# Kernel optimization log

Hardware: AMD Instinct MI355X
Metric: run time of the kernel (lower is better)

The kernel has to match this reference:

```python
import jax, jax.numpy as jnp
import numpy as np

P_ASEM = 0.6


def setup_inputs() -> dict:
    key = jax.random.key(0)
    k1, k2, k3 = jax.random.split(key, 3)
    B, N, D = 8, 2048, 512
    x = jax.random.normal(k1, (B, N, D), dtype=jnp.float32)
    adj = jax.random.uniform(k2, (B, N, N), dtype=jnp.float32)
    # nn.Linear(2D, 1): weight [1, 2D], bias [1]
    bound = 1.0 / np.sqrt(2 * D)
    W = jax.random.uniform(k3, (1, 2 * D), dtype=jnp.float32, minval=-bound, maxval=bound)
    b = jnp.zeros((1,), dtype=jnp.float32)
    return {"x": x, "adj": adj, "W": W, "b": b}


def reference(x, adj, W, b):
    # Faithful to: sigmoid(Linear(cat(xi, xj))) with xi=x[:, i], xj=x[:, j].
    # Split W = [Wi | Wj] so Linear(cat) = x_i @ Wi.T + x_j @ Wj.T + b,
    # avoiding the O(B*N^2*2D) concat intermediate.
    D = x.shape[-1]
    Wi = W[:, :D]  # [1, D]
    Wj = W[:, D:]  # [1, D]
    si = jnp.einsum('bnd,d->bn', x, Wi[0])  # [B, N]
    sj = jnp.einsum('bnd,d->bn', x, Wj[0])  # [B, N]
    xij = jax.nn.sigmoid(si[:, :, None] + sj[:, None, :] + b[0])  # [B, N, N]
    return P_ASEM * xij + (1.0 - P_ASEM) * adj
```

## Files before the change

### kernel.cpp

```cpp
#include <hip/hip_runtime.h>
#include <hip/hip_bf16.h>

#define PB 8
#define PN 2048
#define PD 512
#define P_ASEM 0.6f

typedef float v4f __attribute__((ext_vector_type(4)));

__global__ __launch_bounds__(256) void row_dots_kernel(
    const float* __restrict__ x,
    const float* __restrict__ W,
    float* __restrict__ si,
    float* __restrict__ sj)
{
    const int wave = threadIdx.x >> 6;
    const int lane = threadIdx.x & 63;
    const int row  = blockIdx.x * 4 + wave;

    const v4f* xr = (const v4f*)(x + (size_t)row * PD);
    const v4f* Wi = (const v4f*)(W);
    const v4f* Wj = (const v4f*)(W + PD);

    v4f a0  = __builtin_nontemporal_load(xr + lane);
    v4f a1  = __builtin_nontemporal_load(xr + lane + 64);
    v4f wi0 = Wi[lane];
    v4f wi1 = Wi[lane + 64];
    v4f wj0 = Wj[lane];
    v4f wj1 = Wj[lane + 64];

    float acc_i = a0.x*wi0.x + a0.y*wi0.y + a0.z*wi0.z + a0.w*wi0.w
                + a1.x*wi1.x + a1.y*wi1.y + a1.z*wi1.z + a1.w*wi1.w;
    float acc_j = a0.x*wj0.x + a0.y*wj0.y + a0.z*wj0.z + a0.w*wj0.w
                + a1.x*wj1.x + a1.y*wj1.y + a1.z*wj1.z + a1.w*wj1.w;

    #pragma unroll
    for (int off = 32; off > 0; off >>= 1) {
        acc_i += __shfl_down(acc_i, off, 64);
        acc_j += __shfl_down(acc_j, off, 64);
    }
    if (lane == 0) {
        si[row] = acc_i;
        sj[row] = acc_j;
    }
}

__device__ __forceinline__ float fsigmoid(float t) {
    return __frcp_rn(1.0f + __expf(-t));
}

__global__ __launch_bounds__(256) void blend_kernel(
    const float* __restrict__ adj,
    const float* __restrict__ si,
    const float* __restrict__ sj,
    const float* __restrict__ bptr,
    float* __restrict__ out)
{
    const size_t base = (size_t)blockIdx.x * 1024 + threadIdx.x;
    const float bias = bptr[0];

    size_t idx[4];
    v4f av[4];
    #pragma unroll
    for (int k = 0; k < 4; ++k) {
        idx[k] = base + (size_t)k * 256;
        av[k] = __builtin_nontemporal_load((const v4f*)adj + idx[k]);
    }

    #pragma unroll
    for (int k = 0; k < 4; ++k) {
        const int row  = (int)(idx[k] >> 9);
        const int jc   = (int)(idx[k] & 511);
        const int bidx = row >> 11;
        const float s  = si[row] + bias;
        const v4f sv   = ((const v4f*)(sj + (size_t)bidx * PN))[jc];

        v4f r;
        r.x = P_ASEM * fsigmoid(s + sv.x) + (1.0f - P_ASEM) * av[k].x;
        r.y = P_ASEM * fsigmoid(s + sv.y) + (1.0f - P_ASEM) * av[k].y;
        r.z = P_ASEM * fsigmoid(s + sv.z) + (1.0f - P_ASEM) * av[k].z;
        r.w = P_ASEM * fsigmoid(s + sv.w) + (1.0f - P_ASEM) * av[k].w;
        __builtin_nontemporal_store(r, (v4f*)out + idx[k]);
    }
}

extern "C" void kernel_launch(void* const* d_in, const int* in_sizes, int n_in,
                              void* d_out, int out_size, void* d_ws, size_t ws_size,
                              hipStream_t stream) {
    const float* x   = (const float*)d_in[0];
    const float* adj = (const float*)d_in[1];
    const float* W   = (const float*)d_in[2];
    const float* b   = (const float*)d_in[3];
    float* out = (float*)d_out;

    float* si = (float*)d_ws;
    float* sj = si + (PB * PN);

    row_dots_kernel<<<(PB * PN) / 4, 256, 0, stream>>>(x, W, si, sj);

    const size_t nblocks = (size_t)PB * PN * PN / 4 / 1024;
    blend_kernel<<<(int)nblocks, 256, 0, stream>>>(adj, si, sj, b, out);
}
```

Measured before the change: 242.5 us.

## Factor sigmoid exponentials per row/column and process four rows per block

Sigmoid(si+sj+b) is rewritten as 1/(1+exp(-si-b)*exp(-sj)), so the exponentials are computed once per row and column in the row-dot kernel. The blend kernel then needs only an FMA and a hardware reciprocal per element. Each block now covers four full rows with eight loads per thread, and reuses the column factors across those rows, cutting per-element index math and exp work. The product of two exponentials can overflow or underflow for large logits, and the raw rcp is less exact than before. The kernel remains bound by memory bandwidth on adj and out.

```diff
diff --git a/kernel.cpp b/kernel.cpp
--- a/kernel.cpp
+++ b/kernel.cpp
@@ -1,5 +1,4 @@
 #include <hip/hip_runtime.h>
-#include <hip/hip_bf16.h>
 
 #define PB 8
 #define PN 2048
@@ -11,8 +10,9 @@
 __global__ __launch_bounds__(256) void row_dots_kernel(
     const float* __restrict__ x,
     const float* __restrict__ W,
-    float* __restrict__ si,
-    float* __restrict__ sj)
+    const float* __restrict__ bptr,
+    float* __restrict__ esi,
+    float* __restrict__ esj)
 {
     const int wave = threadIdx.x >> 6;
     const int lane = threadIdx.x & 63;
@@ -40,48 +40,54 @@
         acc_j += __shfl_down(acc_j, off, 64);
     }
     if (lane == 0) {
-        si[row] = acc_i;
-        sj[row] = acc_j;
+        esi[row] = __expf(-(acc_i + bptr[0]));
+        esj[row] = __expf(-acc_j);
     }
 }
 
-__device__ __forceinline__ float fsigmoid(float t) {
-    return __frcp_rn(1.0f + __expf(-t));
+__device__ __forceinline__ v4f blend4(float sr, v4f ej, v4f a) {
+    v4f r;
+    r.x = fmaf(P_ASEM, __builtin_amdgcn_rcpf(fmaf(sr, ej.x, 1.0f)), (1.0f - P_ASEM) * a.x);
+    r.y = fmaf(P_ASEM, __builtin_amdgcn_rcpf(fmaf(sr, ej.y, 1.0f)), (1.0f - P_ASEM) * a.y);
+    r.z = fmaf(P_ASEM, __builtin_amdgcn_rcpf(fmaf(sr, ej.z, 1.0f)), (1.0f - P_ASEM) * a.z);
+    r.w = fmaf(P_ASEM, __builtin_amdgcn_rcpf(fmaf(sr, ej.w, 1.0f)), (1.0f - P_ASEM) * a.w);
+    return r;
 }
 
 __global__ __launch_bounds__(256) void blend_kernel(
     const float* __restrict__ adj,
-    const float* __restrict__ si,
-    const float* __restrict__ sj,
-    const float* __restrict__ bptr,
+    const float* __restrict__ esi,
+    const float* __restrict__ esj,
     float* __restrict__ out)
 {
-    const size_t base = (size_t)blockIdx.x * 1024 + threadIdx.x;
-    const float bias = bptr[0];
+    const int tid = threadIdx.x;
+    const size_t base = (size_t)blockIdx.x * 2048 + tid;
+    const int r0   = blockIdx.x * 4;
+    const int bidx = r0 >> 11;
 
-    size_t idx[4];
-    v4f av[4];
+    v4f av[8];
     #pragma unroll
-    for (int k = 0; k < 4; ++k) {
-        idx[k] = base + (size_t)k * 256;
-        av[k] = __builtin_nontemporal_load((const v4f*)adj + idx[k]);
-    }
+    for (int k = 0; k < 8; ++k)
+        av[k] = __builtin_nontemporal_load((const v4f*)adj + base + (size_t)(k * 256));
 
-    #pragma unroll
-    for (int k = 0; k < 4; ++k) {
-        const int row  = (int)(idx[k] >> 9);
-        const int jc   = (int)(idx[k] & 511);
-        const int bidx = row >> 11;
-        const float s  = si[row] + bias;
-        const v4f sv   = ((const v4f*)(sj + (size_t)bidx * PN))[jc];
+    const v4f* ejb = (const v4f*)esj + (size_t)bidx * (PN / 4);
+    const v4f e0 = ejb[tid];
+    const v4f e1 = ejb[tid + 256];
 
-        v4f r;
-        r.x = P_ASEM * fsigmoid(s + sv.x) + (1.0f - P_ASEM) * av[k].x;
-        r.y = P_ASEM * fsigmoid(s + sv.y) + (1.0f - P_ASEM) * av[k].y;
-        r.z = P_ASEM * fsigmoid(s + sv.z) + (1.0f - P_ASEM) * av[k].z;
-        r.w = P_ASEM * fsigmoid(s + sv.w) + (1.0f - P_ASEM) * av[k].w;
-        __builtin_nontemporal_store(r, (v4f*)out + idx[k]);
-    }
+    const float s0 = esi[r0 + 0];
+    const float s1 = esi[r0 + 1];
+    const float s2 = esi[r0 + 2];
+    const float s3 = esi[r0 + 3];
+
+    v4f* o = (v4f*)out;
+    __builtin_nontemporal_store(blend4(s0, e0, av[0]), o + base + 0 * 256);
+    __builtin_nontemporal_store(blend4(s0, e1, av[1]), o + base + 1 * 256);
+    __builtin_nontemporal_store(blend4(s1, e0, av[2]), o + base + 2 * 256);
+    __builtin_nontemporal_store(blend4(s1, e1, av[3]), o + base + 3 * 256);
+    __builtin_nontemporal_store(blend4(s2, e0, av[4]), o + base + 4 * 256);
+    __builtin_nontemporal_store(blend4(s2, e1, av[5]), o + base + 5 * 256);
+    __builtin_nontemporal_store(blend4(s3, e0, av[6]), o + base + 6 * 256);
+    __builtin_nontemporal_store(blend4(s3, e1, av[7]), o + base + 7 * 256);
 }
 
 extern "C" void kernel_launch(void* const* d_in, const int* in_sizes, int n_in,
@@ -93,11 +99,11 @@
     const float* b   = (const float*)d_in[3];
     float* out = (float*)d_out;
 
-    float* si = (float*)d_ws;
-    float* sj = si + (PB * PN);
+    float* esi = (float*)d_ws;
+    float* esj = esi + (PB * PN);
 
-    row_dots_kernel<<<(PB * PN) / 4, 256, 0, stream>>>(x, W, si, sj);
+    row_dots_kernel<<<(PB * PN) / 4, 256, 0, stream>>>(x, W, b, esi, esj);
 
-    const size_t nblocks = (size_t)PB * PN * PN / 4 / 1024;
-    blend_kernel<<<(int)nblocks, 256, 0, stream>>>(adj, si, sj, b, out);
+    const int nblocks = (int)((size_t)PB * PN * PN / 4 / 2048);
+    blend_kernel<<<nblocks, 256, 0, stream>>>(adj, esi, esj, out);
 }
```

After: 242.3 us. No clear change (-0.1%).
